# Optimization experiments

Hardware: AMD Instinct MI355X
Metric: run time of the kernel (lower is better)

The kernel has to match this reference:

```python
import jax, jax.numpy as jnp
import numpy as np

VOCAB, EMB, HID = 32000, 64, 64
B, S = 16, 256


def setup_inputs() -> dict:
    key = jax.random.key(0)
    ks = jax.random.split(key, 8)
    sc_e = 1.0  # torch nn.Embedding default init is N(0,1)
    sc = 1.0 / np.sqrt(HID)
    emb = jax.random.normal(ks[0], (VOCAB, EMB), jnp.float32) * sc_e
    emb = emb.at[0].set(0.0)  # padding_idx=0
    tokens = jax.random.randint(ks[1], (B, S), 0, VOCAB)
    w_ih = jax.random.normal(ks[2], (3 * HID, EMB), jnp.float32) * sc
    w_hh = jax.random.normal(ks[3], (3 * HID, HID), jnp.float32) * sc
    b_ih = jax.random.normal(ks[4], (3 * HID,), jnp.float32) * sc
    b_hh = jax.random.normal(ks[5], (3 * HID,), jnp.float32) * sc
    w_out = jax.random.normal(ks[6], (VOCAB, HID), jnp.float32) * sc
    b_out = jax.random.normal(ks[7], (VOCAB,), jnp.float32) * sc
    return {"tokens": tokens, "emb": emb, "w_ih": w_ih, "w_hh": w_hh,
            "b_ih": b_ih, "b_hh": b_hh, "w_out": w_out, "b_out": b_out}


def _gru_seq(x, w_ih, w_hh, b_ih, b_hh):
    # x: [B, S, E] -> hidden states [B, S, H]. PyTorch gate order: r, z, n.
    H = w_hh.shape[1]
    xp = jnp.einsum('bse,ge->bsg', x, w_ih) + b_ih  # [B, S, 3H] precomputed

    def step(h, xt):
        hp = h @ w_hh.T + b_hh                      # [B, 3H]
        xr, xz, xn = jnp.split(xt, 3, axis=-1)
        hr, hz, hn = jnp.split(hp, 3, axis=-1)
        r = jax.nn.sigmoid(xr + hr)
        z = jax.nn.sigmoid(xz + hz)
        n = jnp.tanh(xn + r * hn)
        h_new = (1.0 - z) * n + z * h
        return h_new, h_new

    h0 = jnp.zeros((x.shape[0], H), dtype=x.dtype)
    _, hs = jax.lax.scan(step, h0, jnp.swapaxes(xp, 0, 1))  # [S, B, H]
    return jnp.swapaxes(hs, 0, 1)


def reference(tokens, emb, w_ih, w_hh, b_ih, b_hh, w_out, b_out):
    x = emb[tokens]                                  # [B, S, E] embedding lookup
    h = _gru_seq(x, w_ih, w_hh, b_ih, b_hh)          # [B, S, H]
    return h @ w_out.T + b_out                       # [B, S, VOCAB] logits
```

## Files before the change

kernel.cpp:

```cpp
#include <hip/hip_runtime.h>
#include <hip/hip_bf16.h>

#define VOCAB 32000
#define EMB   64
#define HID   64
#define NB    16
#define NS    256
#define G3    192
#define MT    4

typedef __bf16 bf16x8  __attribute__((ext_vector_type(8)));
typedef short  short8  __attribute__((ext_vector_type(8)));
typedef short  short4v __attribute__((ext_vector_type(4)));
typedef float  floatx4 __attribute__((ext_vector_type(4)));
typedef float  floatx2 __attribute__((ext_vector_type(2)));

__device__ __forceinline__ float bf2f(__hip_bfloat16 v) { return __bfloat162float(v); }

__device__ __forceinline__ short f2bf_bits(float f) {
    unsigned int u = __float_as_uint(f);
    unsigned int r = (u + 0x7FFFu + ((u >> 16) & 1u)) >> 16;
    return (short)r;
}

__device__ __forceinline__ bool detect_bf16(const void* p) {
    const unsigned int* w = (const unsigned int*)p;
    unsigned int word = w[threadIdx.x & 63];
    unsigned int e = (word >> 7) & 0xFFu;
    int pred = (e >= 115u) && (e <= 130u);
    unsigned long long m = __ballot(pred);
    return __popcll(m) > 32;
}

__device__ __forceinline__ float bcastf(float v, int l) {
    return __uint_as_float(__builtin_amdgcn_readlane(__float_as_uint(v), l));
}

__global__ __launch_bounds__(G3) void k_embed_proj_t(
    const int* __restrict__ tokens,
    const void* __restrict__ emb_raw,
    const void* __restrict__ w_ih_raw,
    const void* __restrict__ b_ih_raw,
    float* __restrict__ xpt)
{
    const bool isbf = detect_bf16(w_ih_raw);
    const int s   = blockIdx.x;
    const int tid = threadIdx.x;

    __shared__ int   tok_s[NB];
    __shared__ float e_s[NB][EMB];

    if (tid < NB) tok_s[tid] = tokens[tid * NS + s];
    __syncthreads();
    for (int idx = tid; idx < NB * EMB; idx += G3) {
        const int b = idx >> 6, e = idx & 63;
        const int t = tok_s[b];
        e_s[b][e] = isbf ? bf2f(((const __hip_bfloat16*)emb_raw)[t * EMB + e])
                         : ((const float*)emb_raw)[t * EMB + e];
    }
    __syncthreads();

    float wf[EMB];
    if (isbf) {
        const __hip_bfloat16* wrow = (const __hip_bfloat16*)w_ih_raw + tid * EMB;
#pragma unroll
        for (int k0 = 0; k0 < EMB; k0 += 8) {
            bf16x8 wv = *reinterpret_cast<const bf16x8*>(wrow + k0);
#pragma unroll
            for (int j = 0; j < 8; ++j) wf[k0 + j] = (float)wv[j];
        }
    } else {
        const float* wrow = (const float*)w_ih_raw + tid * EMB;
#pragma unroll
        for (int k0 = 0; k0 < EMB; k0 += 4) {
            floatx4 wv = *reinterpret_cast<const floatx4*>(wrow + k0);
#pragma unroll
            for (int j = 0; j < 4; ++j) wf[k0 + j] = wv[j];
        }
    }
    const float bias = isbf ? bf2f(((const __hip_bfloat16*)b_ih_raw)[tid])
                            : ((const float*)b_ih_raw)[tid];

    const int gam = tid >> 6;
    const int u   = tid & 63;
    float* orow = xpt + ((size_t)(s * 3 + gam) * NB) * HID + u;
    for (int b = 0; b < NB; ++b) {
        float acc = bias;
#pragma unroll
        for (int k0 = 0; k0 < EMB; k0 += 4) {
            floatx4 e4 = *reinterpret_cast<const floatx4*>(&e_s[b][k0]);
            acc += e4[0] * wf[k0] + e4[1] * wf[k0 + 1]
                 + e4[2] * wf[k0 + 2] + e4[3] * wf[k0 + 3];
        }
        orow[b * HID] = acc;
    }
}

__global__ __launch_bounds__(64, 1) void k_gru_scan(
    const float* __restrict__ xpt,
    const void* __restrict__ w_hh_raw,
    const void* __restrict__ b_hh_raw,
    __hip_bfloat16* __restrict__ hs)
{
    const bool isbf = detect_bf16(w_hh_raw);
    const int b = blockIdx.x;
    const int j = threadIdx.x;

    floatx2 wr2[HID / 2], wz2[HID / 2], wn2[HID / 2];
    if (isbf) {
        const __hip_bfloat16* w = (const __hip_bfloat16*)w_hh_raw;
#pragma unroll
        for (int k0 = 0; k0 < HID; k0 += 8) {
            bf16x8 v0 = *reinterpret_cast<const bf16x8*>(w + (          j) * HID + k0);
            bf16x8 v1 = *reinterpret_cast<const bf16x8*>(w + (HID     + j) * HID + k0);
            bf16x8 v2 = *reinterpret_cast<const bf16x8*>(w + (2 * HID + j) * HID + k0);
#pragma unroll
            for (int t = 0; t < 4; ++t) {
                wr2[(k0 >> 1) + t] = (floatx2){(float)v0[2 * t], (float)v0[2 * t + 1]};
                wz2[(k0 >> 1) + t] = (floatx2){(float)v1[2 * t], (float)v1[2 * t + 1]};
                wn2[(k0 >> 1) + t] = (floatx2){(float)v2[2 * t], (float)v2[2 * t + 1]};
            }
        }
    } else {
        const float* w = (const float*)w_hh_raw;
#pragma unroll
        for (int k0 = 0; k0 < HID; k0 += 4) {
            floatx4 v0 = *reinterpret_cast<const floatx4*>(w + (          j) * HID + k0);
            floatx4 v1 = *reinterpret_cast<const floatx4*>(w + (HID     + j) * HID + k0);
            floatx4 v2 = *reinterpret_cast<const floatx4*>(w + (2 * HID + j) * HID + k0);
#pragma unroll
            for (int t = 0; t < 2; ++t) {
                wr2[(k0 >> 1) + t] = (floatx2){v0[2 * t], v0[2 * t + 1]};
                wz2[(k0 >> 1) + t] = (floatx2){v1[2 * t], v1[2 * t + 1]};
                wn2[(k0 >> 1) + t] = (floatx2){v2[2 * t], v2[2 * t + 1]};
            }
        }
    }

    float bhr, bhz, bhn;
    if (isbf) {
        const __hip_bfloat16* bb = (const __hip_bfloat16*)b_hh_raw;
        bhr = bf2f(bb[j]); bhz = bf2f(bb[HID + j]); bhn = bf2f(bb[2 * HID + j]);
    } else {
        const float* bb = (const float*)b_hh_raw;
        bhr = bb[j]; bhz = bb[HID + j]; bhn = bb[2 * HID + j];
    }

    const float* xbase = xpt + (size_t)b * HID + j;
#define XLD(s, g) xbase[((size_t)((s) * 3 + (g)) * NB) * HID]

    float xc0 = XLD(0, 0), xc1 = XLD(0, 1), xc2 = XLD(0, 2);
    float xn0 = XLD(1, 0), xn1 = XLD(1, 1), xn2 = XLD(1, 2);
    float h = 0.f;

    for (int s = 0; s < NS; ++s) {
        float pf0 = 0.f, pf1 = 0.f, pf2 = 0.f;
        if (s + 2 < NS) {
            pf0 = XLD(s + 2, 0); pf1 = XLD(s + 2, 1); pf2 = XLD(s + 2, 2);
        }

        floatx2 ar0 = {0.f, 0.f}, ar1 = {0.f, 0.f};
        floatx2 az0 = {0.f, 0.f}, az1 = {0.f, 0.f};
        floatx2 an0 = {0.f, 0.f}, an1 = {0.f, 0.f};
#pragma unroll
        for (int kk = 0; kk < HID; kk += 16) {
            float hb[16];
#pragma unroll
            for (int t = 0; t < 16; ++t) hb[t] = bcastf(h, kk + t);
#pragma unroll
            for (int p = 0; p < 8; ++p) {
                const int w = (kk >> 1) + p;
                floatx2 hv;
                hv[0] = hb[2 * p];
                hv[1] = hb[2 * p + 1];
                if (p & 1) { ar1 += hv * wr2[w]; az1 += hv * wz2[w]; an1 += hv * wn2[w]; }
                else       { ar0 += hv * wr2[w]; az0 += hv * wz2[w]; an0 += hv * wn2[w]; }
            }
        }
        const float arf = (ar0[0] + ar0[1]) + (ar1[0] + ar1[1]);
        const float azf = (az0[0] + az0[1]) + (az1[0] + az1[1]);
        const float anf = (an0[0] + an0[1]) + (an1[0] + an1[1]);

        const float r = __fdividef(1.f, 1.f + __expf(-(xc0 + arf + bhr)));
        const float z = __fdividef(1.f, 1.f + __expf(-(xc1 + azf + bhz)));
        const float n = __fdividef(2.f, 1.f + __expf(-2.f * (xc2 + r * (anf + bhn)))) - 1.f;
        h = (1.f - z) * n + z * h;

        hs[((size_t)b * NS + s) * HID + j] = __float2bfloat16(h);

        xc0 = xn0; xc1 = xn1; xc2 = xn2;
        xn0 = pf0; xn1 = pf1; xn2 = pf2;
    }
#undef XLD
}

__global__ __launch_bounds__(256) void k_logits(
    const __hip_bfloat16* __restrict__ hs,
    const void* __restrict__ w_out_raw,
    const void* __restrict__ b_out_raw,
    void* __restrict__ out_raw)
{
    const bool isbf = detect_bf16(w_out_raw);
    const int mg    = blockIdx.x;
    const int ncb   = blockIdx.y;
    const int wave  = threadIdx.x >> 6;
    const int lane  = threadIdx.x & 63;
    const int quad  = lane >> 4;
    const int l15   = lane & 15;

    __shared__ float tile[4][16][68];

    const int ncol_wave = ncb * 256 + wave * 64;

    bf16x8 B0[4], B1[4];
    float biasv[4];
#pragma unroll
    for (int t = 0; t < 4; ++t) {
        const int ncol = ncol_wave + t * 16;
        if (isbf) {
            const __hip_bfloat16* brow = (const __hip_bfloat16*)w_out_raw + (ncol + l15) * HID;
            B0[t] = *reinterpret_cast<const bf16x8*>(brow + quad * 8);
            B1[t] = *reinterpret_cast<const bf16x8*>(brow + 32 + quad * 8);
            biasv[t] = bf2f(((const __hip_bfloat16*)b_out_raw)[ncol + l15]);
        } else {
            const float* browf = (const float*)w_out_raw + (ncol + l15) * HID;
            floatx4 f0 = *reinterpret_cast<const floatx4*>(browf + quad * 8);
            floatx4 f1 = *reinterpret_cast<const floatx4*>(browf + quad * 8 + 4);
            floatx4 f2 = *reinterpret_cast<const floatx4*>(browf + 32 + quad * 8);
            floatx4 f3 = *reinterpret_cast<const floatx4*>(browf + 32 + quad * 8 + 4);
            short8 s0, s1;
#pragma unroll
            for (int jj = 0; jj < 4; ++jj) {
                s0[jj] = f2bf_bits(f0[jj]); s0[4 + jj] = f2bf_bits(f1[jj]);
                s1[jj] = f2bf_bits(f2[jj]); s1[4 + jj] = f2bf_bits(f3[jj]);
            }
            B0[t] = __builtin_bit_cast(bf16x8, s0);
            B1[t] = __builtin_bit_cast(bf16x8, s1);
            biasv[t] = ((const float*)b_out_raw)[ncol + l15];
        }
    }

#pragma unroll
    for (int mt = 0; mt < MT; ++mt) {
        const int mtile = mg * MT + mt;
        const __hip_bfloat16* arow = hs + (mtile * 16 + l15) * HID;
        const bf16x8 a0 = *reinterpret_cast<const bf16x8*>(arow + quad * 8);
        const bf16x8 a1 = *reinterpret_cast<const bf16x8*>(arow + 32 + quad * 8);

#pragma unroll
        for (int t = 0; t < 4; ++t) {
            floatx4 acc = {0.f, 0.f, 0.f, 0.f};
            acc = __builtin_amdgcn_mfma_f32_16x16x32_bf16(a0, B0[t], acc, 0, 0, 0);
            acc = __builtin_amdgcn_mfma_f32_16x16x32_bf16(a1, B1[t], acc, 0, 0, 0);
#pragma unroll
            for (int i = 0; i < 4; ++i)
                tile[wave][quad * 4 + i][t * 16 + l15] = acc[i] + biasv[t];
        }
        __syncthreads();

        if (isbf) {
            short* outb = (short*)out_raw;
#pragma unroll
            for (int p = 0; p < 4; ++p) {
                const int row = p * 4 + quad;
                const float* src = &tile[wave][row][l15 * 4];
                short4v u;
#pragma unroll
                for (int jj = 0; jj < 4; ++jj) u[jj] = f2bf_bits(src[jj]);
                __builtin_nontemporal_store(u, reinterpret_cast<short4v*>(
                    outb + (size_t)(mtile * 16 + row) * VOCAB + ncol_wave + l15 * 4));
            }
        } else {
            float* outf = (float*)out_raw;
#pragma unroll
            for (int p = 0; p < 4; ++p) {
                const int row = p * 4 + quad;
                floatx4 v = *reinterpret_cast<const floatx4*>(&tile[wave][row][l15 * 4]);
                __builtin_nontemporal_store(v, reinterpret_cast<floatx4*>(
                    outf + (size_t)(mtile * 16 + row) * VOCAB + ncol_wave + l15 * 4));
            }
        }
        __syncthreads();
    }
}

extern "C" void kernel_launch(void* const* d_in, const int* in_sizes, int n_in,
                              void* d_out, int out_size, void* d_ws, size_t ws_size,
                              hipStream_t stream)
{
    const int*  tokens = (const int*)d_in[0];
    const void* emb    = d_in[1];
    const void* w_ih   = d_in[2];
    const void* w_hh   = d_in[3];
    const void* b_ih   = d_in[4];
    const void* b_hh   = d_in[5];
    const void* w_out  = d_in[6];
    const void* b_out  = d_in[7];

    float* xpt = (float*)d_out;
    __hip_bfloat16* hs = (__hip_bfloat16*)d_ws;

    k_embed_proj_t<<<NS, G3, 0, stream>>>(tokens, emb, w_ih, b_ih, xpt);
    k_gru_scan<<<NB, 64, 0, stream>>>(xpt, w_hh, b_hh, hs);
    dim3 grid3((NB * NS) / (16 * MT), VOCAB / 256);
    k_logits<<<grid3, 256, 0, stream>>>(hs, w_out, b_out, d_out);
}
```

Before: 746.1 us.

## Process two batch rows per GRU scan block and double logits M-tile

The GRU scan kernel now runs each block over two batch sequences at once, sharing the register-resident W_hh weights and interleaving two independent recurrences to add instruction-level parallelism and hide the latency of the serial dependency chain. Grid size halves to 8 blocks. Separately, the logits kernel M-tile count MT is doubled, halving the grid in the M dimension and increasing weight reuse per block. The trade-off is fewer blocks in flight on a large GPU and higher register pressure in both kernels.

```diff
diff --git a/kernel.cpp b/kernel.cpp
--- a/kernel.cpp
+++ b/kernel.cpp
@@ -7,7 +7,7 @@
 #define NB    16
 #define NS    256
 #define G3    192
-#define MT    4
+#define MT    8
 
 typedef __bf16 bf16x8  __attribute__((ext_vector_type(8)));
 typedef short  short8  __attribute__((ext_vector_type(8)));
@@ -103,8 +103,8 @@
     __hip_bfloat16* __restrict__ hs)
 {
     const bool isbf = detect_bf16(w_hh_raw);
-    const int b = blockIdx.x;
-    const int j = threadIdx.x;
+    const int b0 = blockIdx.x * 2;
+    const int j  = threadIdx.x;
 
     floatx2 wr2[HID / 2], wz2[HID / 2], wn2[HID / 2];
     if (isbf) {
@@ -146,52 +146,67 @@
         bhr = bb[j]; bhz = bb[HID + j]; bhn = bb[2 * HID + j];
     }
 
-    const float* xbase = xpt + (size_t)b * HID + j;
-#define XLD(s, g) xbase[((size_t)((s) * 3 + (g)) * NB) * HID]
-
-    float xc0 = XLD(0, 0), xc1 = XLD(0, 1), xc2 = XLD(0, 2);
-    float xn0 = XLD(1, 0), xn1 = XLD(1, 1), xn2 = XLD(1, 2);
-    float h = 0.f;
+    const float* xbA = xpt + (size_t)b0 * HID + j;
+    const float* xbB = xpt + (size_t)(b0 + 1) * HID + j;
+#define XLDA(s, g) xbA[((size_t)((s) * 3 + (g)) * NB) * HID]
+#define XLDB(s, g) xbB[((size_t)((s) * 3 + (g)) * NB) * HID]
+
+    float xcA0 = XLDA(0, 0), xcA1 = XLDA(0, 1), xcA2 = XLDA(0, 2);
+    float xcB0 = XLDB(0, 0), xcB1 = XLDB(0, 1), xcB2 = XLDB(0, 2);
+    float xnA0 = XLDA(1, 0), xnA1 = XLDA(1, 1), xnA2 = XLDA(1, 2);
+    float xnB0 = XLDB(1, 0), xnB1 = XLDB(1, 1), xnB2 = XLDB(1, 2);
+    float hA = 0.f, hB = 0.f;
 
     for (int s = 0; s < NS; ++s) {
-        float pf0 = 0.f, pf1 = 0.f, pf2 = 0.f;
+        float pfA0 = 0.f, pfA1 = 0.f, pfA2 = 0.f;
+        float pfB0 = 0.f, pfB1 = 0.f, pfB2 = 0.f;
         if (s + 2 < NS) {
-            pf0 = XLD(s + 2, 0); pf1 = XLD(s + 2, 1); pf2 = XLD(s + 2, 2);
-        }
-
-        floatx2 ar0 = {0.f, 0.f}, ar1 = {0.f, 0.f};
-        floatx2 az0 = {0.f, 0.f}, az1 = {0.f, 0.f};
-        floatx2 an0 = {0.f, 0.f}, an1 = {0.f, 0.f};
-#pragma unroll
-        for (int kk = 0; kk < HID; kk += 16) {
-            float hb[16];
-#pragma unroll
-            for (int t = 0; t < 16; ++t) hb[t] = bcastf(h, kk + t);
-#pragma unroll
-            for (int p = 0; p < 8; ++p) {
+            pfA0 = XLDA(s + 2, 0); pfA1 = XLDA(s + 2, 1); pfA2 = XLDA(s + 2, 2);
+            pfB0 = XLDB(s + 2, 0); pfB1 = XLDB(s + 2, 1); pfB2 = XLDB(s + 2, 2);
+        }
+
+        floatx2 arA = {0.f, 0.f}, azA = {0.f, 0.f}, anA = {0.f, 0.f};
+        floatx2 arB = {0.f, 0.f}, azB = {0.f, 0.f}, anB = {0.f, 0.f};
+#pragma unroll
+        for (int kk = 0; kk < HID; kk += 8) {
+            float ha[8], hbv[8];
+#pragma unroll
+            for (int t = 0; t < 8; ++t) ha[t]  = bcastf(hA, kk + t);
+#pragma unroll
+            for (int t = 0; t < 8; ++t) hbv[t] = bcastf(hB, kk + t);
+#pragma unroll
+            for (int p = 0; p < 4; ++p) {
                 const int w = (kk >> 1) + p;
-                floatx2 hv;
-                hv[0] = hb[2 * p];
-                hv[1] = hb[2 * p + 1];
-                if (p & 1) { ar1 += hv * wr2[w]; az1 += hv * wz2[w]; an1 += hv * wn2[w]; }
-                else       { ar0 += hv * wr2[w]; az0 += hv * wz2[w]; an0 += hv * wn2[w]; }
-            }
-        }
-        const float arf = (ar0[0] + ar0[1]) + (ar1[0] + ar1[1]);
-        const float azf = (az0[0] + az0[1]) + (az1[0] + az1[1]);
-        const float anf = (an0[0] + an0[1]) + (an1[0] + an1[1]);
-
-        const float r = __fdividef(1.f, 1.f + __expf(-(xc0 + arf + bhr)));
-        const float z = __fdividef(1.f, 1.f + __expf(-(xc1 + azf + bhz)));
-        const float n = __fdividef(2.f, 1.f + __expf(-2.f * (xc2 + r * (anf + bhn)))) - 1.f;
-        h = (1.f - z) * n + z * h;
-
-        hs[((size_t)b * NS + s) * HID + j] = __float2bfloat16(h);
-
-        xc0 = xn0; xc1 = xn1; xc2 = xn2;
-        xn0 = pf0; xn1 = pf1; xn2 = pf2;
-    }
-#undef XLD
+                floatx2 hvA, hvB;
+                hvA[0] = ha[2 * p];  hvA[1] = ha[2 * p + 1];
+                hvB[0] = hbv[2 * p]; hvB[1] = hbv[2 * p + 1];
+                arA += hvA * wr2[w]; arB += hvB * wr2[w];
+                azA += hvA * wz2[w]; azB += hvB * wz2[w];
+                anA += hvA * wn2[w]; anB += hvB * wn2[w];
+            }
+        }
+        const float arfA = arA[0] + arA[1], azfA = azA[0] + azA[1], anfA = anA[0] + anA[1];
+        const float arfB = arB[0] + arB[1], azfB = azB[0] + azB[1], anfB = anB[0] + anB[1];
+
+        const float rA = __fdividef(1.f, 1.f + __expf(-(xcA0 + arfA + bhr)));
+        const float rB = __fdividef(1.f, 1.f + __expf(-(xcB0 + arfB + bhr)));
+        const float zA = __fdividef(1.f, 1.f + __expf(-(xcA1 + azfA + bhz)));
+        const float zB = __fdividef(1.f, 1.f + __expf(-(xcB1 + azfB + bhz)));
+        const float nA = __fdividef(2.f, 1.f + __expf(-2.f * (xcA2 + rA * (anfA + bhn)))) - 1.f;
+        const float nB = __fdividef(2.f, 1.f + __expf(-2.f * (xcB2 + rB * (anfB + bhn)))) - 1.f;
+        hA = (1.f - zA) * nA + zA * hA;
+        hB = (1.f - zB) * nB + zB * hB;
+
+        hs[((size_t)b0 * NS + s) * HID + j]       = __float2bfloat16(hA);
+        hs[((size_t)(b0 + 1) * NS + s) * HID + j] = __float2bfloat16(hB);
+
+        xcA0 = xnA0; xcA1 = xnA1; xcA2 = xnA2;
+        xcB0 = xnB0; xcB1 = xnB1; xcB2 = xnB2;
+        xnA0 = pfA0; xnA1 = pfA1; xnA2 = pfA2;
+        xnB0 = pfB0; xnB1 = pfB1; xnB2 = pfB2;
+    }
+#undef XLDA
+#undef XLDB
 }
 
 __global__ __launch_bounds__(256) void k_logits(
@@ -301,7 +316,7 @@
     __hip_bfloat16* hs = (__hip_bfloat16*)d_ws;
 
     k_embed_proj_t<<<NS, G3, 0, stream>>>(tokens, emb, w_ih, b_ih, xpt);
-    k_gru_scan<<<NB, 64, 0, stream>>>(xpt, w_hh, b_hh, hs);
+    k_gru_scan<<<NB / 2, 64, 0, stream>>>(xpt, w_hh, b_hh, hs);
     dim3 grid3((NB * NS) / (16 * MT), VOCAB / 256);
     k_logits<<<grid3, 256, 0, stream>>>(hs, w_out, b_out, d_out);
 }
```

Result: slower. 799.2 us (+7.1%).
